# Kernel optimization log

Measured on AMD Instinct MI355X. Metric: run time of the kernel, lower is better.

## Reference

```python
import jax, jax.numpy as jnp
import numpy as np

EMB = 1024
HEADS = 16
HEAD_DIM = EMB // HEADS
SEQ = 2048
BATCH = 2
FF = 4 * EMB


def gelu_tanh(x):
    # matches the hand-rolled GELU: 0.5*x*(1+tanh(sqrt(2/pi)*(x+0.044715*x^3)))
    c = jnp.sqrt(jnp.asarray(2.0 / jnp.pi, dtype=x.dtype))
    return 0.5 * x * (1.0 + jnp.tanh(c * (x + 0.044715 * x ** 3)))


def layernorm(x, scale, shift, eps=1e-5):
    mean = jnp.mean(x, axis=-1, keepdims=True)
    var = jnp.var(x, axis=-1, keepdims=True)  # unbiased=False
    return scale * (x - mean) * jax.lax.rsqrt(var + eps) + shift


def setup_inputs() -> dict:
    key = jax.random.key(0)
    ks = jax.random.split(key, 10)
    s = 1.0 / np.sqrt(EMB)
    sf = 1.0 / np.sqrt(FF)
    return {
        "x": jax.random.normal(ks[0], (BATCH, SEQ, EMB), jnp.float32),
        "Wq": jax.random.uniform(ks[1], (EMB, EMB), jnp.float32, -s, s),
        "Wk": jax.random.uniform(ks[2], (EMB, EMB), jnp.float32, -s, s),
        "Wv": jax.random.uniform(ks[3], (EMB, EMB), jnp.float32, -s, s),
        "Wo": jax.random.uniform(ks[4], (EMB, EMB), jnp.float32, -s, s),
        "bo": jnp.zeros((EMB,), jnp.float32),
        "ln1_g": jnp.ones((EMB,), jnp.float32),
        "ln1_b": jnp.zeros((EMB,), jnp.float32),
        "ln2_g": jnp.ones((EMB,), jnp.float32),
        "ln2_b": jnp.zeros((EMB,), jnp.float32),
        "W1": jax.random.uniform(ks[5], (EMB, FF), jnp.float32, -s, s),
        "b1": jnp.zeros((FF,), jnp.float32),
        "W2": jax.random.uniform(ks[6], (FF, EMB), jnp.float32, -sf, sf),
        "b2": jnp.zeros((EMB,), jnp.float32),
    }


def reference(x, Wq, Wk, Wv, Wo, bo, ln1_g, ln1_b, ln2_g, ln2_b, W1, b1, W2, b2):
    b, n, d = x.shape
    shortcut = x
    h = layernorm(x, ln1_g, ln1_b)
    # projections -> [b, heads, n, head_dim]
    def split_heads(t):
        return t.reshape(b, n, HEADS, HEAD_DIM).transpose(0, 2, 1, 3)
    q = split_heads(h @ Wq)
    k = split_heads(h @ Wk)
    v = split_heads(h @ Wv)
    scores = jnp.einsum("bhqd,bhkd->bhqk", q, k)
    causal = jnp.triu(jnp.ones((n, n), dtype=bool), k=1)
    scores = jnp.where(causal, -jnp.inf, scores)
    weights = jax.nn.softmax(scores / jnp.sqrt(jnp.asarray(HEAD_DIM, x.dtype)), axis=-1)
    ctx = jnp.einsum("bhqk,bhkd->bhqd", weights, v)
    ctx = ctx.transpose(0, 2, 1, 3).reshape(b, n, d)
    attn_out = ctx @ Wo + bo
    x = attn_out + shortcut
    shortcut = x
    h = layernorm(x, ln2_g, ln2_b)
    ff = gelu_tanh(h @ W1 + b1) @ W2 + b2
    return ff + shortcut
```

## Files before the change

kernel.cpp:

```cpp
#include <hip/hip_runtime.h>

typedef __bf16 bf16x8 __attribute__((ext_vector_type(8)));
typedef float f32x4 __attribute__((ext_vector_type(4)));
typedef unsigned short u16;

#define EMB 1024
#define SEQ 2048
#define BATCH 2
#define HEADS 16
#define HEAD_DIM 64
#define FF 4096
#define ROWS (BATCH * SEQ)

static __device__ __forceinline__ u16 f2bf(float f) {
    unsigned int u = __builtin_bit_cast(unsigned int, f);
    unsigned int r = (u + 0x7FFFu + ((u >> 16) & 1u)) >> 16;
    return (u16)r;
}

static __device__ __forceinline__ void gload16(const u16* g, u16* l) {
    __builtin_amdgcn_global_load_lds(
        (const __attribute__((address_space(1))) unsigned int*)(const void*)g,
        (__attribute__((address_space(3))) unsigned int*)(void*)l, 16, 0, 0);
}

__global__ __launch_bounds__(256) void transpose_f32_to_bf16(
    const float* __restrict__ in, u16* __restrict__ out, int R, int C) {
    __shared__ float tile[32][33];
    int c0 = blockIdx.x * 32, r0 = blockIdx.y * 32;
    int tx = threadIdx.x & 31, ty = threadIdx.x >> 5;
#pragma unroll
    for (int i = 0; i < 32; i += 8)
        tile[ty + i][tx] = in[(size_t)(r0 + ty + i) * C + c0 + tx];
    __syncthreads();
#pragma unroll
    for (int i = 0; i < 32; i += 8)
        out[(size_t)(c0 + ty + i) * R + r0 + tx] = f2bf(tile[tx][ty + i]);
}

__global__ __launch_bounds__(256) void ln_kernel(
    const float* __restrict__ x, const float* __restrict__ gamma,
    const float* __restrict__ beta, u16* __restrict__ out) {
    int row = blockIdx.x;
    int t = threadIdx.x;
    float4 v = reinterpret_cast<const float4*>(x + (size_t)row * EMB)[t];
    float s = v.x + v.y + v.z + v.w;
    float s2 = v.x * v.x + v.y * v.y + v.z * v.z + v.w * v.w;
#pragma unroll
    for (int off = 1; off < 64; off <<= 1) {
        s += __shfl_xor(s, off);
        s2 += __shfl_xor(s2, off);
    }
    __shared__ float sm[8];
    int wid = t >> 6;
    if ((t & 63) == 0) { sm[wid] = s; sm[wid + 4] = s2; }
    __syncthreads();
    s = sm[0] + sm[1] + sm[2] + sm[3];
    s2 = sm[4] + sm[5] + sm[6] + sm[7];
    float mean = s * (1.0f / EMB);
    float var = s2 * (1.0f / EMB) - mean * mean;
    float inv = rsqrtf(var + 1e-5f);
    float4 gv = reinterpret_cast<const float4*>(gamma)[t];
    float4 bv = reinterpret_cast<const float4*>(beta)[t];
    ushort4 o;
    o.x = f2bf((v.x - mean) * inv * gv.x + bv.x);
    o.y = f2bf((v.y - mean) * inv * gv.y + bv.y);
    o.z = f2bf((v.z - mean) * inv * gv.z + bv.z);
    o.w = f2bf((v.w - mean) * inv * gv.w + bv.w);
    reinterpret_cast<ushort4*>(out + (size_t)row * EMB)[t] = o;
}

template <int EPI>
__global__ __launch_bounds__(256) void gemm_bf16(
    const u16* __restrict__ A, const u16* __restrict__ B, void* __restrict__ Cout,
    const float* __restrict__ bias, const float* __restrict__ resid,
    void* __restrict__ Cout2, void* __restrict__ Cout3,
    int M, int N, int K) {
    __shared__ u16 As[128 * 64];
    __shared__ u16 Bs[128 * 64];
    int tm = blockIdx.x * 128;
    int tn = blockIdx.y * 128;
    int t = threadIdx.x;
    int lane = t & 63, wid = t >> 6;
    int wr = (wid >> 1) * 64, wc = (wid & 1) * 64;
    int l15 = lane & 15, g = lane >> 4;
    const u16* Abase = A + (size_t)tm * K;
    const u16* Bbase = B + (size_t)tn * K;
    f32x4 acc[4][4] = {};
    for (int k0 = 0; k0 < K; k0 += 64) {
        __syncthreads();
#pragma unroll
        for (int p = 0; p < 4; ++p) {
            int chunk = (wid * 4 + p) * 64 + lane;
            int row = chunk >> 3, c8 = (chunk & 7) * 8;
            gload16(Abase + (size_t)row * K + k0 + c8, &As[(wid * 4 + p) * 512]);
            gload16(Bbase + (size_t)row * K + k0 + c8, &Bs[(wid * 4 + p) * 512]);
        }
        __syncthreads();
#pragma unroll
        for (int kc = 0; kc < 2; ++kc) {
            int ko = kc * 32 + g * 8;
            bf16x8 af[4], bfr[4];
#pragma unroll
            for (int i = 0; i < 4; ++i)
                af[i] = *reinterpret_cast<const bf16x8*>(&As[(wr + i * 16 + l15) * 64 + ko]);
#pragma unroll
            for (int j = 0; j < 4; ++j)
                bfr[j] = *reinterpret_cast<const bf16x8*>(&Bs[(wc + j * 16 + l15) * 64 + ko]);
#pragma unroll
            for (int i = 0; i < 4; ++i)
#pragma unroll
                for (int j = 0; j < 4; ++j)
                    acc[i][j] = __builtin_amdgcn_mfma_f32_16x16x32_bf16(af[i], bfr[j], acc[i][j], 0, 0, 0);
        }
    }
    int mb = tm + wr + g * 4;
    int nb = tn + wc + l15;
#pragma unroll
    for (int i = 0; i < 4; ++i) {
#pragma unroll
        for (int j = 0; j < 4; ++j) {
            int n = nb + j * 16;
#pragma unroll
            for (int r = 0; r < 4; ++r) {
                int m = mb + i * 16 + r;
                float val = acc[i][j][r];
                if constexpr (EPI == 0) {
                    ((u16*)Cout)[(size_t)m * N + n] = f2bf(val);
                } else if constexpr (EPI == 1) {
                    ((float*)Cout)[(size_t)m * N + n] =
                        val + bias[n] + resid[(size_t)m * N + n];
                } else if constexpr (EPI == 2) {
                    float xg = val + bias[n];
                    float x3 = xg + 0.044715f * xg * xg * xg;
                    float tz = 0.7978845608028654f * x3;
                    float th = 1.0f - 2.0f / (1.0f + __expf(2.0f * tz));
                    ((u16*)Cout)[(size_t)m * N + n] = f2bf(0.5f * xg * (1.0f + th));
                } else {
                    if (n < 1024) {
                        ((u16*)Cout)[(size_t)m * 1024 + n] = f2bf(val);
                    } else if (n < 2048) {
                        ((u16*)Cout2)[(size_t)m * 1024 + (n - 1024)] = f2bf(val);
                    } else {
                        int bb = m >> 11, ss = m & 2047;
                        ((u16*)Cout3)[((size_t)(bb * EMB + (n - 2048))) * SEQ + ss] = f2bf(val);
                    }
                }
            }
        }
    }
}

__global__ __launch_bounds__(64) void attn_kernel(
    const u16* __restrict__ Qb, const u16* __restrict__ Kb,
    const u16* __restrict__ Vt, u16* __restrict__ ctx) {
    __shared__ u16 P_lds[32][72];
    int bh = blockIdx.x;
    int b = bh >> 4, h = bh & 15;
    int qc = 63 - (int)blockIdx.y;
    int lane = threadIdx.x;
    int l15 = lane & 15, g = lane >> 4;
    int qbase = qc * 32;

    bf16x8 qf[2][2];
#pragma unroll
    for (int qt = 0; qt < 2; ++qt)
#pragma unroll
        for (int kc = 0; kc < 2; ++kc)
            qf[qt][kc] = *reinterpret_cast<const bf16x8*>(
                Qb + (size_t)(b * SEQ + qbase + qt * 16 + l15) * EMB + h * 64 + kc * 32 + g * 8);

    f32x4 ctx_acc[2][4] = {};
    float mrun[2] = {-1e30f, -1e30f};
    float lrun[2] = {0.f, 0.f};
    int nkt = qc / 2 + 1;

    for (int kt = 0; kt < nkt; ++kt) {
        int k0 = kt * 64;
        f32x4 sacc[4][2] = {};
#pragma unroll
        for (int kc = 0; kc < 2; ++kc) {
#pragma unroll
            for (int ktile = 0; ktile < 4; ++ktile) {
                bf16x8 kf = *reinterpret_cast<const bf16x8*>(
                    Kb + (size_t)(b * SEQ + k0 + ktile * 16 + l15) * EMB + h * 64 + kc * 32 + g * 8);
#pragma unroll
                for (int qt = 0; qt < 2; ++qt)
                    sacc[ktile][qt] = __builtin_amdgcn_mfma_f32_16x16x32_bf16(
                        kf, qf[qt][kc], sacc[ktile][qt], 0, 0, 0);
            }
        }
#pragma unroll
        for (int qt = 0; qt < 2; ++qt) {
            int q = qbase + qt * 16 + l15;
            float sv[16];
            float tmax = -1e30f;
#pragma unroll
            for (int ktile = 0; ktile < 4; ++ktile)
#pragma unroll
                for (int r = 0; r < 4; ++r) {
                    int key = k0 + ktile * 16 + g * 4 + r;
                    float sx = sacc[ktile][qt][r] * 0.125f;
                    if (key > q) sx = -1e30f;
                    sv[ktile * 4 + r] = sx;
                    tmax = fmaxf(tmax, sx);
                }
            tmax = fmaxf(tmax, __shfl_xor(tmax, 16));
            tmax = fmaxf(tmax, __shfl_xor(tmax, 32));
            float mnew = fmaxf(mrun[qt], tmax);
            float corr = __expf(mrun[qt] - mnew);
            mrun[qt] = mnew;
            float psum = 0.f;
#pragma unroll
            for (int idx = 0; idx < 16; ++idx) {
                float p = __expf(sv[idx] - mnew);
                sv[idx] = p;
                psum += p;
            }
            lrun[qt] = lrun[qt] * corr + psum;
            float corr4[4];
#pragma unroll
            for (int r = 0; r < 4; ++r) corr4[r] = __shfl(corr, g * 4 + r);
#pragma unroll
            for (int dt = 0; dt < 4; ++dt)
#pragma unroll
                for (int r = 0; r < 4; ++r) ctx_acc[qt][dt][r] *= corr4[r];
#pragma unroll
            for (int ktile = 0; ktile < 4; ++ktile) {
                ushort4 pk;
                pk.x = f2bf(sv[ktile * 4 + 0]);
                pk.y = f2bf(sv[ktile * 4 + 1]);
                pk.z = f2bf(sv[ktile * 4 + 2]);
                pk.w = f2bf(sv[ktile * 4 + 3]);
                *reinterpret_cast<ushort4*>(&P_lds[qt * 16 + l15][ktile * 16 + g * 4]) = pk;
            }
        }
        asm volatile("s_waitcnt lgkmcnt(0)" ::: "memory");
#pragma unroll
        for (int kc = 0; kc < 2; ++kc) {
            bf16x8 pf[2];
#pragma unroll
            for (int qt = 0; qt < 2; ++qt)
                pf[qt] = *reinterpret_cast<const bf16x8*>(&P_lds[qt * 16 + l15][kc * 32 + g * 8]);
#pragma unroll
            for (int dt = 0; dt < 4; ++dt) {
                bf16x8 vf = *reinterpret_cast<const bf16x8*>(
                    Vt + (size_t)(b * EMB + h * 64 + dt * 16 + l15) * SEQ + k0 + kc * 32 + g * 8);
#pragma unroll
                for (int qt = 0; qt < 2; ++qt)
                    ctx_acc[qt][dt] = __builtin_amdgcn_mfma_f32_16x16x32_bf16(
                        pf[qt], vf, ctx_acc[qt][dt], 0, 0, 0);
            }
        }
    }
#pragma unroll
    for (int qt = 0; qt < 2; ++qt) {
        float lsum = lrun[qt];
        lsum += __shfl_xor(lsum, 16);
        lsum += __shfl_xor(lsum, 32);
        float d4[4];
#pragma unroll
        for (int r = 0; r < 4; ++r) d4[r] = __shfl(lsum, g * 4 + r);
#pragma unroll
        for (int dt = 0; dt < 4; ++dt)
#pragma unroll
            for (int r = 0; r < 4; ++r) {
                int q = qbase + qt * 16 + g * 4 + r;
                int d = h * 64 + dt * 16 + l15;
                ctx[(size_t)(b * SEQ + q) * EMB + d] = f2bf(ctx_acc[qt][dt][r] / d4[r]);
            }
    }
}

extern "C" void kernel_launch(void* const* d_in, const int* in_sizes, int n_in,
                              void* d_out, int out_size, void* d_ws, size_t ws_size,
                              hipStream_t stream) {
    const float* x    = (const float*)d_in[0];
    const float* Wq   = (const float*)d_in[1];
    const float* Wk   = (const float*)d_in[2];
    const float* Wv   = (const float*)d_in[3];
    const float* Wo   = (const float*)d_in[4];
    const float* bo   = (const float*)d_in[5];
    const float* ln1g = (const float*)d_in[6];
    const float* ln1b = (const float*)d_in[7];
    const float* ln2g = (const float*)d_in[8];
    const float* ln2b = (const float*)d_in[9];
    const float* W1   = (const float*)d_in[10];
    const float* b1   = (const float*)d_in[11];
    const float* W2   = (const float*)d_in[12];
    const float* b2   = (const float*)d_in[13];

    char* ws = (char*)d_ws;
    size_t off = 0;
    auto alloc = [&](size_t bytes) {
        void* p = ws + off;
        off += (bytes + 255) & ~(size_t)255;
        return p;
    };
    u16* h1     = (u16*)alloc((size_t)ROWS * EMB * 2);
    u16* Wqkvt  = (u16*)alloc((size_t)3 * EMB * EMB * 2);
    u16* Wot    = (u16*)alloc((size_t)EMB * EMB * 2);
    u16* W1t    = (u16*)alloc((size_t)FF * EMB * 2);
    u16* W2t    = (u16*)alloc((size_t)EMB * FF * 2);
    u16* Qb     = (u16*)alloc((size_t)ROWS * EMB * 2);
    u16* Kb     = (u16*)alloc((size_t)ROWS * EMB * 2);
    u16* Vtb    = (u16*)alloc((size_t)BATCH * EMB * SEQ * 2);
    u16* ctxb   = (u16*)alloc((size_t)ROWS * EMB * 2);
    float* x2   = (float*)alloc((size_t)ROWS * EMB * 4);
    u16* h2     = (u16*)alloc((size_t)ROWS * EMB * 2);
    u16* ff1    = (u16*)alloc((size_t)ROWS * FF * 2);

    u16* Wqt = Wqkvt;
    u16* Wkt = Wqkvt + (size_t)EMB * EMB;
    u16* Wvt = Wqkvt + (size_t)2 * EMB * EMB;

    transpose_f32_to_bf16<<<dim3(32, 32), 256, 0, stream>>>(Wq, Wqt, EMB, EMB);
    transpose_f32_to_bf16<<<dim3(32, 32), 256, 0, stream>>>(Wk, Wkt, EMB, EMB);
    transpose_f32_to_bf16<<<dim3(32, 32), 256, 0, stream>>>(Wv, Wvt, EMB, EMB);
    transpose_f32_to_bf16<<<dim3(32, 32), 256, 0, stream>>>(Wo, Wot, EMB, EMB);
    transpose_f32_to_bf16<<<dim3(128, 32), 256, 0, stream>>>(W1, W1t, EMB, FF);
    transpose_f32_to_bf16<<<dim3(32, 128), 256, 0, stream>>>(W2, W2t, FF, EMB);

    ln_kernel<<<ROWS, 256, 0, stream>>>(x, ln1g, ln1b, h1);

    gemm_bf16<4><<<dim3(32, 24), 256, 0, stream>>>(h1, Wqkvt, Qb, nullptr, nullptr,
                                                   Kb, Vtb, ROWS, 3072, EMB);

    attn_kernel<<<dim3(32, 64), 64, 0, stream>>>(Qb, Kb, Vtb, ctxb);

    gemm_bf16<1><<<dim3(32, 8), 256, 0, stream>>>(ctxb, Wot, x2, bo, x,
                                                  nullptr, nullptr, ROWS, EMB, EMB);

    ln_kernel<<<ROWS, 256, 0, stream>>>(x2, ln2g, ln2b, h2);

    gemm_bf16<2><<<dim3(32, 32), 256, 0, stream>>>(h2, W1t, ff1, b1, nullptr,
                                                   nullptr, nullptr, ROWS, FF, EMB);
    gemm_bf16<1><<<dim3(32, 8), 256, 0, stream>>>(ff1, W2t, (float*)d_out, b2, x2,
                                                  nullptr, nullptr, ROWS, EMB, FF);
}
```

Baseline: 481.0 us.

## Prefetch K/V tiles, skip masking and rescale, prescale Q, batch weight transposes

The attention kernel now double-buffers K fragments in registers and loads V fragments before the QK MFMAs, so global-load latency can overlap compute. It folds the 1/sqrt(d) scale into Q, applies the causal mask only on the final diagonal tile, and skips the running-max rescale unless the new max exceeds the old one by more than a threshold. P is also packed to bf16 by truncation with a byte permute rather than round-to-nearest. The four square weight transposes are merged into one launch. In exchange, register pressure rises, and truncation plus lazy rescaling slightly change numerics.

Result: faster. 437.1 us (-9.1%).

```diff
diff --git a/kernel.cpp b/kernel.cpp
--- a/kernel.cpp
+++ b/kernel.cpp
@@ -18,6 +18,11 @@
     return (u16)r;
 }
 
+static __device__ __forceinline__ unsigned int pack_bf_trunc(float a, float b) {
+    return __builtin_amdgcn_perm(__builtin_bit_cast(unsigned int, a),
+                                 __builtin_bit_cast(unsigned int, b), 0x07060302u);
+}
+
 static __device__ __forceinline__ void gload16(const u16* g, u16* l) {
     __builtin_amdgcn_global_load_lds(
         (const __attribute__((address_space(1))) unsigned int*)(const void*)g,
@@ -36,6 +41,31 @@
 #pragma unroll
     for (int i = 0; i < 32; i += 8)
         out[(size_t)(c0 + ty + i) * R + r0 + tx] = f2bf(tile[tx][ty + i]);
+}
+
+__global__ __launch_bounds__(256) void transpose4_f32_to_bf16(
+    const float* __restrict__ s0, const float* __restrict__ s1,
+    const float* __restrict__ s2, const float* __restrict__ s3,
+    u16* __restrict__ d0, u16* __restrict__ d1,
+    u16* __restrict__ d2, u16* __restrict__ d3) {
+    __shared__ float tile[32][33];
+    const float* in;
+    u16* out;
+    switch (blockIdx.z) {
+        case 0: in = s0; out = d0; break;
+        case 1: in = s1; out = d1; break;
+        case 2: in = s2; out = d2; break;
+        default: in = s3; out = d3; break;
+    }
+    int c0 = blockIdx.x * 32, r0 = blockIdx.y * 32;
+    int tx = threadIdx.x & 31, ty = threadIdx.x >> 5;
+#pragma unroll
+    for (int i = 0; i < 32; i += 8)
+        tile[ty + i][tx] = in[(size_t)(r0 + ty + i) * EMB + c0 + tx];
+    __syncthreads();
+#pragma unroll
+    for (int i = 0; i < 32; i += 8)
+        out[(size_t)(c0 + ty + i) * EMB + r0 + tx] = f2bf(tile[tx][ty + i]);
 }
 
 __global__ __launch_bounds__(256) void ln_kernel(
@@ -162,77 +192,118 @@
     int l15 = lane & 15, g = lane >> 4;
     int qbase = qc * 32;
 
+    const u16* Qrow = Qb + (size_t)(b * SEQ) * EMB + h * 64;
+    const u16* Krow = Kb + (size_t)(b * SEQ) * EMB + h * 64;
+    const u16* Vrow = Vt + (size_t)(b * EMB + h * 64) * SEQ;
+
     bf16x8 qf[2][2];
 #pragma unroll
     for (int qt = 0; qt < 2; ++qt)
 #pragma unroll
-        for (int kc = 0; kc < 2; ++kc)
-            qf[qt][kc] = *reinterpret_cast<const bf16x8*>(
-                Qb + (size_t)(b * SEQ + qbase + qt * 16 + l15) * EMB + h * 64 + kc * 32 + g * 8);
+        for (int kc = 0; kc < 2; ++kc) {
+            bf16x8 v = *reinterpret_cast<const bf16x8*>(
+                Qrow + (size_t)(qbase + qt * 16 + l15) * EMB + kc * 32 + g * 8);
+            bf16x8 sv;
+#pragma unroll
+            for (int e = 0; e < 8; ++e) sv[e] = (__bf16)((float)v[e] * 0.125f);
+            qf[qt][kc] = sv;
+        }
 
     f32x4 ctx_acc[2][4] = {};
     float mrun[2] = {-1e30f, -1e30f};
     float lrun[2] = {0.f, 0.f};
     int nkt = qc / 2 + 1;
 
+    bf16x8 kcur[8], knxt[8];
+#pragma unroll
+    for (int i = 0; i < 8; ++i) {
+        int kc = i >> 2, ktile = i & 3;
+        kcur[i] = *reinterpret_cast<const bf16x8*>(
+            Krow + (size_t)(ktile * 16 + l15) * EMB + kc * 32 + g * 8);
+    }
+
     for (int kt = 0; kt < nkt; ++kt) {
         int k0 = kt * 64;
+        bool last = (kt == nkt - 1);
+        bf16x8 vf[8];
+#pragma unroll
+        for (int i = 0; i < 8; ++i) {
+            int kc = i >> 2, dt = i & 3;
+            vf[i] = *reinterpret_cast<const bf16x8*>(
+                Vrow + (size_t)(dt * 16 + l15) * SEQ + k0 + kc * 32 + g * 8);
+        }
         f32x4 sacc[4][2] = {};
 #pragma unroll
-        for (int kc = 0; kc < 2; ++kc) {
-#pragma unroll
-            for (int ktile = 0; ktile < 4; ++ktile) {
-                bf16x8 kf = *reinterpret_cast<const bf16x8*>(
-                    Kb + (size_t)(b * SEQ + k0 + ktile * 16 + l15) * EMB + h * 64 + kc * 32 + g * 8);
+        for (int kc = 0; kc < 2; ++kc)
+#pragma unroll
+            for (int ktile = 0; ktile < 4; ++ktile)
 #pragma unroll
                 for (int qt = 0; qt < 2; ++qt)
                     sacc[ktile][qt] = __builtin_amdgcn_mfma_f32_16x16x32_bf16(
-                        kf, qf[qt][kc], sacc[ktile][qt], 0, 0, 0);
+                        kcur[kc * 4 + ktile], qf[qt][kc], sacc[ktile][qt], 0, 0, 0);
+        if (kt + 1 < nkt) {
+#pragma unroll
+            for (int i = 0; i < 8; ++i) {
+                int kc = i >> 2, ktile = i & 3;
+                knxt[i] = *reinterpret_cast<const bf16x8*>(
+                    Krow + (size_t)(k0 + 64 + ktile * 16 + l15) * EMB + kc * 32 + g * 8);
             }
         }
 #pragma unroll
         for (int qt = 0; qt < 2; ++qt) {
-            int q = qbase + qt * 16 + l15;
             float sv[16];
             float tmax = -1e30f;
-#pragma unroll
-            for (int ktile = 0; ktile < 4; ++ktile)
-#pragma unroll
-                for (int r = 0; r < 4; ++r) {
-                    int key = k0 + ktile * 16 + g * 4 + r;
-                    float sx = sacc[ktile][qt][r] * 0.125f;
-                    if (key > q) sx = -1e30f;
-                    sv[ktile * 4 + r] = sx;
-                    tmax = fmaxf(tmax, sx);
-                }
+            if (last) {
+                int q = qbase + qt * 16 + l15;
+#pragma unroll
+                for (int ktile = 0; ktile < 4; ++ktile)
+#pragma unroll
+                    for (int r = 0; r < 4; ++r) {
+                        int key = k0 + ktile * 16 + g * 4 + r;
+                        float sx = (key > q) ? -1e30f : sacc[ktile][qt][r];
+                        sv[ktile * 4 + r] = sx;
+                        tmax = fmaxf(tmax, sx);
+                    }
+            } else {
+#pragma unroll
+                for (int ktile = 0; ktile < 4; ++ktile)
+#pragma unroll
+                    for (int r = 0; r < 4; ++r) {
+                        float sx = sacc[ktile][qt][r];
+                        sv[ktile * 4 + r] = sx;
+                        tmax = fmaxf(tmax, sx);
+                    }
+            }
             tmax = fmaxf(tmax, __shfl_xor(tmax, 16));
             tmax = fmaxf(tmax, __shfl_xor(tmax, 32));
-            float mnew = fmaxf(mrun[qt], tmax);
-            float corr = __expf(mrun[qt] - mnew);
-            mrun[qt] = mnew;
+            if (!__all(tmax <= mrun[qt] + 8.0f)) {
+                float mnew = fmaxf(mrun[qt], tmax);
+                float corr = __expf(mrun[qt] - mnew);
+                mrun[qt] = mnew;
+                lrun[qt] *= corr;
+                float corr4[4];
+#pragma unroll
+                for (int r = 0; r < 4; ++r) corr4[r] = __shfl(corr, g * 4 + r);
+#pragma unroll
+                for (int dt = 0; dt < 4; ++dt)
+#pragma unroll
+                    for (int r = 0; r < 4; ++r) ctx_acc[qt][dt][r] *= corr4[r];
+            }
+            float m = mrun[qt];
             float psum = 0.f;
 #pragma unroll
             for (int idx = 0; idx < 16; ++idx) {
-                float p = __expf(sv[idx] - mnew);
+                float p = __expf(sv[idx] - m);
                 sv[idx] = p;
                 psum += p;
             }
-            lrun[qt] = lrun[qt] * corr + psum;
-            float corr4[4];
-#pragma unroll
-            for (int r = 0; r < 4; ++r) corr4[r] = __shfl(corr, g * 4 + r);
-#pragma unroll
-            for (int dt = 0; dt < 4; ++dt)
-#pragma unroll
-                for (int r = 0; r < 4; ++r) ctx_acc[qt][dt][r] *= corr4[r];
+            lrun[qt] += psum;
 #pragma unroll
             for (int ktile = 0; ktile < 4; ++ktile) {
-                ushort4 pk;
-                pk.x = f2bf(sv[ktile * 4 + 0]);
-                pk.y = f2bf(sv[ktile * 4 + 1]);
-                pk.z = f2bf(sv[ktile * 4 + 2]);
-                pk.w = f2bf(sv[ktile * 4 + 3]);
-                *reinterpret_cast<ushort4*>(&P_lds[qt * 16 + l15][ktile * 16 + g * 4]) = pk;
+                uint2 w;
+                w.x = pack_bf_trunc(sv[ktile * 4 + 1], sv[ktile * 4 + 0]);
+                w.y = pack_bf_trunc(sv[ktile * 4 + 3], sv[ktile * 4 + 2]);
+                *reinterpret_cast<uint2*>(&P_lds[qt * 16 + l15][ktile * 16 + g * 4]) = w;
             }
         }
         asm volatile("s_waitcnt lgkmcnt(0)" ::: "memory");
@@ -243,15 +314,14 @@
             for (int qt = 0; qt < 2; ++qt)
                 pf[qt] = *reinterpret_cast<const bf16x8*>(&P_lds[qt * 16 + l15][kc * 32 + g * 8]);
 #pragma unroll
-            for (int dt = 0; dt < 4; ++dt) {
-                bf16x8 vf = *reinterpret_cast<const bf16x8*>(
-                    Vt + (size_t)(b * EMB + h * 64 + dt * 16 + l15) * SEQ + k0 + kc * 32 + g * 8);
+            for (int dt = 0; dt < 4; ++dt)
 #pragma unroll
                 for (int qt = 0; qt < 2; ++qt)
                     ctx_acc[qt][dt] = __builtin_amdgcn_mfma_f32_16x16x32_bf16(
-                        pf[qt], vf, ctx_acc[qt][dt], 0, 0, 0);
-            }
-        }
+                        pf[qt], vf[kc * 4 + dt], ctx_acc[qt][dt], 0, 0, 0);
+        }
+#pragma unroll
+        for (int i = 0; i < 8; ++i) kcur[i] = knxt[i];
     }
 #pragma unroll
     for (int qt = 0; qt < 2; ++qt) {
@@ -314,10 +384,8 @@
     u16* Wkt = Wqkvt + (size_t)EMB * EMB;
     u16* Wvt = Wqkvt + (size_t)2 * EMB * EMB;
 
-    transpose_f32_to_bf16<<<dim3(32, 32), 256, 0, stream>>>(Wq, Wqt, EMB, EMB);
-    transpose_f32_to_bf16<<<dim3(32, 32), 256, 0, stream>>>(Wk, Wkt, EMB, EMB);
-    transpose_f32_to_bf16<<<dim3(32, 32), 256, 0, stream>>>(Wv, Wvt, EMB, EMB);
-    transpose_f32_to_bf16<<<dim3(32, 32), 256, 0, stream>>>(Wo, Wot, EMB, EMB);
+    transpose4_f32_to_bf16<<<dim3(32, 32, 4), 256, 0, stream>>>(
+        Wq, Wk, Wv, Wo, Wqt, Wkt, Wvt, Wot);
     transpose_f32_to_bf16<<<dim3(128, 32), 256, 0, stream>>>(W1, W1t, EMB, FF);
     transpose_f32_to_bf16<<<dim3(32, 128), 256, 0, stream>>>(W2, W2t, FF, EMB);
 
```
